# Kernel tuning notes

Measured on AMD Instinct MI355X. Metric: run time of the kernel, lower is better.

The kernel has to match this reference:

```python
import jax, jax.numpy as jnp
import numpy as np
import math

D_MODEL = 512

def setup_inputs() -> dict:
    key = jax.random.key(0)
    k1, k2, k3 = jax.random.split(key, 3)
    X = jax.random.normal(k1, (4, 8192, D_MODEL), dtype=jnp.float32)
    # nn.Linear(d, d, bias=False) weights, applied as x @ W.T
    s = 1.0 / math.sqrt(D_MODEL)
    W_v = jax.random.uniform(k2, (D_MODEL, D_MODEL), dtype=jnp.float32, minval=-s, maxval=s)
    W_theta = jax.random.uniform(k3, (D_MODEL, D_MODEL), dtype=jnp.float32, minval=-s, maxval=s)
    return {"X": X, "W_v": W_v, "W_theta": W_theta}

def reference(X, W_v, W_theta):
    # X: [B, n, d]
    n = X.shape[1]
    d = X.shape[2]
    XW_v = X @ W_v.T            # [B, n, d]
    theta_X = X @ W_theta.T     # [B, n, d]
    # first term: (1/n) * ones(n,n) @ XW_v == column mean broadcast over rows
    first_term = jnp.mean(XW_v, axis=1, keepdims=True)  # [B, 1, d], broadcasts
    # second term: (1/(n*sqrt(d))) * (X @ theta_X^T) @ XW_v
    # associativity-reduced: theta_X^T @ XW_v is [B, d, d]
    kv = jnp.einsum('bnd,bne->bde', theta_X, XW_v)       # [B, d, d]
    second_term = (X @ kv) / (n * math.sqrt(d))          # [B, n, d]
    return first_term + second_term
```

## Files before the change

### kernel.cpp

```cpp
#include <hip/hip_runtime.h>
#include <stdint.h>


typedef __bf16 bf16x8 __attribute__((ext_vector_type(8)));
typedef float f32x4 __attribute__((ext_vector_type(4)));
typedef unsigned short u16x4 __attribute__((ext_vector_type(4)));
typedef unsigned short u16x8 __attribute__((ext_vector_type(8)));

#define BM 128
#define BN 128
#define BK 32

__device__ __forceinline__ unsigned short f2bf(float f) {
  union { float f; unsigned int u; } c; c.f = f;
  unsigned int u = c.u;
  return (unsigned short)((u + 0x7FFFu + ((u >> 16) & 1u)) >> 16);
}
__device__ __forceinline__ float bf2f(unsigned short h) {
  union { unsigned int u; float f; } c; c.u = ((unsigned int)h) << 16;
  return c.f;
}

__device__ __forceinline__ void gld16(const void* g, void* l) {
  using gptr_t = const __attribute__((address_space(1))) void*;
  using lptr_t = __attribute__((address_space(3))) void*;
  __builtin_amdgcn_global_load_lds((gptr_t)(uintptr_t)g,
                                   (lptr_t)(uint32_t)(uintptr_t)l, 16, 0, 0);
}

__device__ __forceinline__ void gemm_tile(const unsigned short* __restrict__ A, int lda,
                                          const unsigned short* __restrict__ B, int ldb,
                                          int K, int m0, int n0, f32x4 (&acc)[4][4]) {
  __shared__ unsigned short sA[BM * BK];
  __shared__ unsigned short sB[BN * BK];
  const int tid = threadIdx.x;
  const int lane = tid & 63;
  const int w = tid >> 6;
  const int wm = w >> 1, wn = w & 1;
  const int quad = lane >> 4, l16 = lane & 15;

#pragma unroll
  for (int mi = 0; mi < 4; mi++)
#pragma unroll
    for (int ni = 0; ni < 4; ni++) acc[mi][ni] = f32x4{0.f, 0.f, 0.f, 0.f};

  for (int kt = 0; kt < K; kt += BK) {
#pragma unroll
    for (int j = 0; j < 2; j++) {
      const int slot = w * 128 + j * 64 + lane;
      const int row = slot >> 2;
      const int col = (slot & 3) * 8;
      gld16(A + (size_t)(m0 + row) * lda + kt + col,
            (char*)sA + (size_t)(w * 128 + j * 64) * 16);
      gld16(B + (size_t)(n0 + row) * ldb + kt + col,
            (char*)sB + (size_t)(w * 128 + j * 64) * 16);
    }
    __syncthreads();

    bf16x8 af[4], bfr[4];
#pragma unroll
    for (int mi = 0; mi < 4; mi++)
      af[mi] = *(const bf16x8*)&sA[(wm * 64 + mi * 16 + l16) * BK + quad * 8];
#pragma unroll
    for (int ni = 0; ni < 4; ni++)
      bfr[ni] = *(const bf16x8*)&sB[(wn * 64 + ni * 16 + l16) * BK + quad * 8];
#pragma unroll
    for (int mi = 0; mi < 4; mi++)
#pragma unroll
      for (int ni = 0; ni < 4; ni++)
        acc[mi][ni] = __builtin_amdgcn_mfma_f32_16x16x32_bf16(af[mi], bfr[ni],
                                                              acc[mi][ni], 0, 0, 0);
    __syncthreads();
  }
}

__global__ __launch_bounds__(256) void prep_kernel(const float* __restrict__ X,
                                                   unsigned short* __restrict__ Xb,
                                                   unsigned short* __restrict__ Xt) {
  __shared__ unsigned short sT[64 * 64];
  const int t = threadIdx.x;
  const int n0 = blockIdx.x * 64, d0 = blockIdx.y * 64;
  const int b = n0 >> 13, nb = n0 & 8191;
  const int r0 = (t >> 4) * 4, c0 = (t & 15) * 4;
  f32x4 v[4];
#pragma unroll
  for (int i = 0; i < 4; i++)
    v[i] = *(const f32x4*)(X + (size_t)(n0 + r0 + i) * 512 + d0 + c0);
#pragma unroll
  for (int i = 0; i < 4; i++) {
    u16x4 o;
#pragma unroll
    for (int j = 0; j < 4; j++) o[j] = f2bf(v[i][j]);
    *(u16x4*)(Xb + (size_t)(n0 + r0 + i) * 512 + d0 + c0) = o;
  }
#pragma unroll
  for (int j = 0; j < 4; j++) {
    u16x4 w;
#pragma unroll
    for (int i = 0; i < 4; i++) w[i] = f2bf(v[i][j]);
    const int c = c0 + j;
    const int rsw = r0 ^ (c & 0x3c);
    *(u16x4*)&sT[c * 64 + rsw] = w;
  }
  __syncthreads();
  const int c = t >> 2, p = t & 3;
  const int sw = c & 0x3c;
  unsigned short* dst = Xt + (size_t)(b * 512 + d0 + c) * 8192 + nb + p * 16;
#pragma unroll
  for (int q = 0; q < 4; q++)
    *(u16x4*)(dst + q * 4) = *(const u16x4*)&sT[c * 64 + ((p * 16 + q * 4) ^ sw)];
}

static __device__ const int TI[10] = {0, 0, 0, 0, 1, 1, 1, 2, 2, 3};
static __device__ const int TJ[10] = {0, 1, 2, 3, 1, 2, 3, 2, 3, 3};

__global__ __launch_bounds__(256) void g_gemm_kernel(const unsigned short* __restrict__ Xt,
                                                     float* __restrict__ G_part) {
  const int t = blockIdx.x;
  const int z = blockIdx.y;
  const int b = z >> 4, s = z & 15;
  const int m0 = TI[t] * 128, n0 = TJ[t] * 128;
  const unsigned short* A = Xt + (size_t)b * 512 * 8192 + (size_t)s * 512;
  f32x4 acc[4][4];
  gemm_tile(A, 8192, A, 8192, 512, m0, n0, acc);
  float* Cp = G_part + ((size_t)z * 10 + t) * 16384;
  const int tid = threadIdx.x, lane = tid & 63, w = tid >> 6;
  const int wm = w >> 1, wn = w & 1, quad = lane >> 4, l16 = lane & 15;
#pragma unroll
  for (int mi = 0; mi < 4; mi++)
#pragma unroll
    for (int ni = 0; ni < 4; ni++) {
      const int ml = wm * 64 + mi * 16 + quad * 4;
      const int nl = wn * 64 + ni * 16 + l16;
      *(f32x4*)(Cp + (size_t)nl * 128 + ml) = acc[mi][ni];
    }
}

__global__ __launch_bounds__(256) void g_fin_kernel(const float* __restrict__ G_part,
                                                    unsigned short* __restrict__ Gb) {
  const int blk = blockIdx.x;
  const int b = blk / 80, rem = blk % 80;
  const int t = rem >> 3, cc = rem & 7;
  const int i = TI[t], j = TJ[t];
  const int m0 = i * 128, n0 = j * 128;
  const int tid = threadIdx.x;
  const int np = cc * 16 + (tid >> 4);
  const int mp = (tid & 15) * 8;
  f32x4 s0 = f32x4{0.f, 0.f, 0.f, 0.f}, s1 = f32x4{0.f, 0.f, 0.f, 0.f};
#pragma unroll
  for (int s = 0; s < 16; s++) {
    const float* p = G_part + (((size_t)(b * 16 + s)) * 10 + t) * 16384 + (size_t)np * 128 + mp;
    s0 += *(const f32x4*)p;
    s1 += *(const f32x4*)(p + 4);
  }
  const float scale = (float)(1.0 / (8192.0 * 22.627416997969522));
  unsigned short h[8];
#pragma unroll
  for (int r = 0; r < 4; r++) { h[r] = f2bf(s0[r] * scale); h[r + 4] = f2bf(s1[r] * scale); }
  unsigned short* Gbb = Gb + (size_t)b * 262144;
#pragma unroll
  for (int r = 0; r < 8; r++)
    Gbb[(size_t)(m0 + mp + r) * 512 + (n0 + np)] = h[r];
  if (i != j) {
    u16x8 o;
#pragma unroll
    for (int r = 0; r < 8; r++) o[r] = h[r];
    *(u16x8*)(Gbb + (size_t)(n0 + np) * 512 + (m0 + mp)) = o;
  }
}

__global__ __launch_bounds__(256) void gemm_rm_kernel(const unsigned short* __restrict__ A,
                                                      const unsigned short* __restrict__ B,
                                                      unsigned short* __restrict__ C,
                                                      size_t Abs, size_t Bbs) {
  const int b = blockIdx.z;
  const int m0 = blockIdx.x * BM, n0 = blockIdx.y * BN;
  f32x4 acc[4][4];
  gemm_tile(A + (size_t)b * Abs, 512, B + (size_t)b * Bbs, 512, 512, m0, n0, acc);
  unsigned short* Cb = C + (size_t)b * 262144;
  const int tid = threadIdx.x, lane = tid & 63, w = tid >> 6;
  const int wm = w >> 1, wn = w & 1, quad = lane >> 4, l16 = lane & 15;
#pragma unroll
  for (int mi = 0; mi < 4; mi++)
#pragma unroll
    for (int ni = 0; ni < 4; ni++) {
      const int m = m0 + wm * 64 + mi * 16 + quad * 4;
      const int n = n0 + wn * 64 + ni * 16 + l16;
#pragma unroll
      for (int r = 0; r < 4; r++)
        Cb[(size_t)(m + r) * 512 + n] = f2bf(acc[mi][ni][r]);
    }
}

__global__ __launch_bounds__(256) void gemm_out_kernel(
    const unsigned short* __restrict__ Xb, const unsigned short* __restrict__ kvt,
    const float* __restrict__ meanV, float* __restrict__ out) {
  const int m0 = blockIdx.x * BM, n0 = blockIdx.y * BN;
  const int b = blockIdx.x >> 6;
  const unsigned short* Bm = kvt + (size_t)b * 262144;
  f32x4 acc[4][4];
  gemm_tile(Xb, 512, Bm, 512, 512, m0, n0, acc);
  const int tid = threadIdx.x, lane = tid & 63, w = tid >> 6;
  const int wm = w >> 1, wn = w & 1, quad = lane >> 4, l16 = lane & 15;
#pragma unroll
  for (int ni = 0; ni < 4; ni++) {
    const int e = n0 + wn * 64 + ni * 16 + l16;
    const float mu = meanV[b * 512 + e];
#pragma unroll
    for (int mi = 0; mi < 4; mi++) {
      const int m = m0 + wm * 64 + mi * 16 + quad * 4;
#pragma unroll
      for (int r = 0; r < 4; r++)
        out[(size_t)(m + r) * 512 + e] = acc[mi][ni][r] + mu;
    }
  }
}

__global__ __launch_bounds__(256) void cast_kernel(const float* __restrict__ in,
                                                   unsigned short* __restrict__ out,
                                                   int n8) {
  const int i = blockIdx.x * 256 + threadIdx.x;
  if (i >= n8) return;
  const f32x4* p = (const f32x4*)(in + (size_t)i * 8);
  f32x4 v0 = p[0], v1 = p[1];
  u16x8 o;
  o[0] = f2bf(v0[0]); o[1] = f2bf(v0[1]); o[2] = f2bf(v0[2]); o[3] = f2bf(v0[3]);
  o[4] = f2bf(v1[0]); o[5] = f2bf(v1[1]); o[6] = f2bf(v1[2]); o[7] = f2bf(v1[3]);
  *(u16x8*)(out + (size_t)i * 8) = o;
}

__global__ __launch_bounds__(256) void meanx_kernel(const unsigned short* __restrict__ Xt,
                                                    float* __restrict__ mean_x) {
  const int be = blockIdx.x;
  const unsigned short* row = Xt + (size_t)be * 8192;
  const int t = threadIdx.x;
  float s = 0.f;
  for (int c = t; c < 1024; c += 256) {
    u16x8 v = *(const u16x8*)(row + c * 8);
#pragma unroll
    for (int j = 0; j < 8; j++) s += bf2f(v[j]);
  }
  __shared__ float red[256];
  red[t] = s;
  __syncthreads();
  for (int st = 128; st > 0; st >>= 1) {
    if (t < st) red[t] += red[t + st];
    __syncthreads();
  }
  if (t == 0) mean_x[be] = red[0] * (1.f / 8192.f);
}

__global__ __launch_bounds__(256) void meanv_kernel(const float* __restrict__ mean_x,
                                                    const float* __restrict__ Wv,
                                                    float* __restrict__ meanV) {
  const int idx = blockIdx.x * 256 + threadIdx.x;
  const int b = idx >> 9, e = idx & 511;
  const float* mx = mean_x + b * 512;
  const float* wr = Wv + (size_t)e * 512;
  float s = 0.f;
  for (int d = 0; d < 512; d += 4) {
    f32x4 a = *(const f32x4*)(mx + d);
    f32x4 w = *(const f32x4*)(wr + d);
    s += a[0] * w[0] + a[1] * w[1] + a[2] * w[2] + a[3] * w[3];
  }
  meanV[idx] = s;
}

extern "C" void kernel_launch(void* const* d_in, const int* in_sizes, int n_in,
                              void* d_out, int out_size, void* d_ws, size_t ws_size,
                              hipStream_t stream) {
  const float* X = (const float*)d_in[0];
  const float* Wv = (const float*)d_in[1];
  const float* Wth = (const float*)d_in[2];
  float* out = (float*)d_out;
  char* ws = (char*)d_ws;

  unsigned short* Xb = (unsigned short*)(ws);
  unsigned short* Xt = (unsigned short*)(ws + 33554432ull);
  float* G_part = (float*)(ws + 67108864ull);
  unsigned short* Gb = (unsigned short*)(ws + 109051904ull);
  unsigned short* Ht = (unsigned short*)(ws + 111149056ull);
  unsigned short* kvt = (unsigned short*)(ws + 113246208ull);
  unsigned short* Wvb = (unsigned short*)(ws + 115343360ull);
  unsigned short* Wtb = (unsigned short*)(ws + 115867648ull);
  float* mean_x = (float*)(ws + 116391936ull);
  float* meanV = (float*)(ws + 116400128ull);

  prep_kernel<<<dim3(512, 8), 256, 0, stream>>>(X, Xb, Xt);
  cast_kernel<<<128, 256, 0, stream>>>(Wv, Wvb, 32768);
  cast_kernel<<<128, 256, 0, stream>>>(Wth, Wtb, 32768);

  g_gemm_kernel<<<dim3(10, 64), 256, 0, stream>>>(Xt, G_part);
  meanx_kernel<<<2048, 256, 0, stream>>>(Xt, mean_x);
  meanv_kernel<<<8, 256, 0, stream>>>(mean_x, Wv, meanV);
  g_fin_kernel<<<320, 256, 0, stream>>>(G_part, Gb);

  gemm_rm_kernel<<<dim3(4, 4, 4), 256, 0, stream>>>(Wvb, Gb, Ht, 0, 262144);
  gemm_rm_kernel<<<dim3(4, 4, 4), 256, 0, stream>>>(Ht, Wtb, kvt, 262144, 0);

  gemm_out_kernel<<<dim3(256, 4), 256, 0, stream>>>(Xb, kvt, meanV, out);
}
```

Before: 261.8 us.

## Fuse column-mean into prep, merge weight casts, double K-step GEMM tile

The column sums of X are now computed inside the prep kernel with wave shuffles and atomics, which removes the separate meanx pass that re-read Xt. The two weight cast kernels are merged into a single launch that also zeroes the mean accumulator. The prep transpose store is widened to 16-byte writes with a different swizzle. The shared GEMM tile now stages two K-chunks per barrier, and diagonal Gram tiles load their operand only once. The costs are extra LDS per block, atomic contention on the mean buffer, and sums taken in fp32 instead of from the bf16 copy.

```diff
diff --git a/kernel.cpp b/kernel.cpp
--- a/kernel.cpp
+++ b/kernel.cpp
@@ -15,10 +15,6 @@
   union { float f; unsigned int u; } c; c.f = f;
   unsigned int u = c.u;
   return (unsigned short)((u + 0x7FFFu + ((u >> 16) & 1u)) >> 16);
-}
-__device__ __forceinline__ float bf2f(unsigned short h) {
-  union { unsigned int u; float f; } c; c.u = ((unsigned int)h) << 16;
-  return c.f;
 }
 
 __device__ __forceinline__ void gld16(const void* g, void* l) {
@@ -30,9 +26,10 @@
 
 __device__ __forceinline__ void gemm_tile(const unsigned short* __restrict__ A, int lda,
                                           const unsigned short* __restrict__ B, int ldb,
-                                          int K, int m0, int n0, f32x4 (&acc)[4][4]) {
-  __shared__ unsigned short sA[BM * BK];
-  __shared__ unsigned short sB[BN * BK];
+                                          int K, int m0, int n0, f32x4 (&acc)[4][4],
+                                          bool sameAB) {
+  __shared__ unsigned short sA[2][BM * BK];
+  __shared__ unsigned short sB[2][BN * BK];
   const int tid = threadIdx.x;
   const int lane = tid & 63;
   const int w = tid >> 6;
@@ -44,39 +41,49 @@
 #pragma unroll
     for (int ni = 0; ni < 4; ni++) acc[mi][ni] = f32x4{0.f, 0.f, 0.f, 0.f};
 
-  for (int kt = 0; kt < K; kt += BK) {
-#pragma unroll
-    for (int j = 0; j < 2; j++) {
-      const int slot = w * 128 + j * 64 + lane;
-      const int row = slot >> 2;
-      const int col = (slot & 3) * 8;
-      gld16(A + (size_t)(m0 + row) * lda + kt + col,
-            (char*)sA + (size_t)(w * 128 + j * 64) * 16);
-      gld16(B + (size_t)(n0 + row) * ldb + kt + col,
-            (char*)sB + (size_t)(w * 128 + j * 64) * 16);
+  for (int kt = 0; kt < K; kt += 2 * BK) {
+#pragma unroll
+    for (int h = 0; h < 2; h++) {
+#pragma unroll
+      for (int j = 0; j < 2; j++) {
+        const int slot = w * 128 + j * 64 + lane;
+        const int row = slot >> 2;
+        const int col = (slot & 3) * 8;
+        const int kc = kt + h * BK + col;
+        gld16(A + (size_t)(m0 + row) * lda + kc,
+              (char*)sA[h] + (size_t)(w * 128 + j * 64) * 16);
+        if (!sameAB)
+          gld16(B + (size_t)(n0 + row) * ldb + kc,
+                (char*)sB[h] + (size_t)(w * 128 + j * 64) * 16);
+      }
     }
     __syncthreads();
 
-    bf16x8 af[4], bfr[4];
-#pragma unroll
-    for (int mi = 0; mi < 4; mi++)
-      af[mi] = *(const bf16x8*)&sA[(wm * 64 + mi * 16 + l16) * BK + quad * 8];
-#pragma unroll
-    for (int ni = 0; ni < 4; ni++)
-      bfr[ni] = *(const bf16x8*)&sB[(wn * 64 + ni * 16 + l16) * BK + quad * 8];
-#pragma unroll
-    for (int mi = 0; mi < 4; mi++)
+#pragma unroll
+    for (int h = 0; h < 2; h++) {
+      const unsigned short* bs = sameAB ? sA[h] : sB[h];
+      bf16x8 af[4], bfr[4];
+#pragma unroll
+      for (int mi = 0; mi < 4; mi++)
+        af[mi] = *(const bf16x8*)&sA[h][(wm * 64 + mi * 16 + l16) * BK + quad * 8];
 #pragma unroll
       for (int ni = 0; ni < 4; ni++)
-        acc[mi][ni] = __builtin_amdgcn_mfma_f32_16x16x32_bf16(af[mi], bfr[ni],
-                                                              acc[mi][ni], 0, 0, 0);
+        bfr[ni] = *(const bf16x8*)&bs[(wn * 64 + ni * 16 + l16) * BK + quad * 8];
+#pragma unroll
+      for (int mi = 0; mi < 4; mi++)
+#pragma unroll
+        for (int ni = 0; ni < 4; ni++)
+          acc[mi][ni] = __builtin_amdgcn_mfma_f32_16x16x32_bf16(af[mi], bfr[ni],
+                                                                acc[mi][ni], 0, 0, 0);
+    }
     __syncthreads();
   }
 }
 
 __global__ __launch_bounds__(256) void prep_kernel(const float* __restrict__ X,
                                                    unsigned short* __restrict__ Xb,
-                                                   unsigned short* __restrict__ Xt) {
+                                                   unsigned short* __restrict__ Xt,
+                                                   float* __restrict__ mean_acc) {
   __shared__ unsigned short sT[64 * 64];
   const int t = threadIdx.x;
   const int n0 = blockIdx.x * 64, d0 = blockIdx.y * 64;
@@ -93,22 +100,61 @@
     for (int j = 0; j < 4; j++) o[j] = f2bf(v[i][j]);
     *(u16x4*)(Xb + (size_t)(n0 + r0 + i) * 512 + d0 + c0) = o;
   }
+  float cs[4];
+#pragma unroll
+  for (int j = 0; j < 4; j++) cs[j] = v[0][j] + v[1][j] + v[2][j] + v[3][j];
 #pragma unroll
   for (int j = 0; j < 4; j++) {
-    u16x4 w;
-#pragma unroll
-    for (int i = 0; i < 4; i++) w[i] = f2bf(v[i][j]);
+    cs[j] += __shfl_xor(cs[j], 16);
+    cs[j] += __shfl_xor(cs[j], 32);
+  }
+  if ((t & 63) < 16) {
+#pragma unroll
+    for (int j = 0; j < 4; j++)
+      atomicAdd(mean_acc + b * 512 + d0 + c0 + j, cs[j]);
+  }
+#pragma unroll
+  for (int j = 0; j < 4; j++) {
+    u16x4 wv;
+#pragma unroll
+    for (int i = 0; i < 4; i++) wv[i] = f2bf(v[i][j]);
     const int c = c0 + j;
-    const int rsw = r0 ^ (c & 0x3c);
-    *(u16x4*)&sT[c * 64 + rsw] = w;
+    const int rsw = r0 ^ (c & 0x38);
+    *(u16x4*)&sT[c * 64 + rsw] = wv;
   }
   __syncthreads();
-  const int c = t >> 2, p = t & 3;
-  const int sw = c & 0x3c;
-  unsigned short* dst = Xt + (size_t)(b * 512 + d0 + c) * 8192 + nb + p * 16;
-#pragma unroll
-  for (int q = 0; q < 4; q++)
-    *(u16x4*)(dst + q * 4) = *(const u16x4*)&sT[c * 64 + ((p * 16 + q * 4) ^ sw)];
+  const int cr = t >> 3, p = t & 7;
+#pragma unroll
+  for (int h = 0; h < 2; h++) {
+    const int c = cr + h * 32;
+    const int phys = (p * 8) ^ (c & 0x38);
+    u16x8 val = *(const u16x8*)&sT[c * 64 + phys];
+    *(u16x8*)(Xt + (size_t)(b * 512 + d0 + c) * 8192 + nb + p * 8) = val;
+  }
+}
+
+__global__ __launch_bounds__(256) void prep_w_kernel(const float* __restrict__ Wv,
+                                                     const float* __restrict__ Wth,
+                                                     unsigned short* __restrict__ Wvb,
+                                                     unsigned short* __restrict__ Wtb,
+                                                     float* __restrict__ mean_acc) {
+  const int blk = blockIdx.x;
+  const int t = threadIdx.x;
+  if (blk == 256) {
+    f32x4 z = f32x4{0.f, 0.f, 0.f, 0.f};
+    *(f32x4*)(mean_acc + t * 8) = z;
+    *(f32x4*)(mean_acc + t * 8 + 4) = z;
+    return;
+  }
+  const float* src = (blk < 128) ? Wv : Wth;
+  unsigned short* dst = (blk < 128) ? Wvb : Wtb;
+  const int i = (blk & 127) * 256 + t;
+  const f32x4* pp = (const f32x4*)(src + (size_t)i * 8);
+  f32x4 v0 = pp[0], v1 = pp[1];
+  u16x8 o;
+  o[0] = f2bf(v0[0]); o[1] = f2bf(v0[1]); o[2] = f2bf(v0[2]); o[3] = f2bf(v0[3]);
+  o[4] = f2bf(v1[0]); o[5] = f2bf(v1[1]); o[6] = f2bf(v1[2]); o[7] = f2bf(v1[3]);
+  *(u16x8*)(dst + (size_t)i * 8) = o;
 }
 
 static __device__ const int TI[10] = {0, 0, 0, 0, 1, 1, 1, 2, 2, 3};
@@ -122,7 +168,7 @@
   const int m0 = TI[t] * 128, n0 = TJ[t] * 128;
   const unsigned short* A = Xt + (size_t)b * 512 * 8192 + (size_t)s * 512;
   f32x4 acc[4][4];
-  gemm_tile(A, 8192, A, 8192, 512, m0, n0, acc);
+  gemm_tile(A, 8192, A, 8192, 512, m0, n0, acc, m0 == n0);
   float* Cp = G_part + ((size_t)z * 10 + t) * 16384;
   const int tid = threadIdx.x, lane = tid & 63, w = tid >> 6;
   const int wm = w >> 1, wn = w & 1, quad = lane >> 4, l16 = lane & 15;
@@ -176,7 +222,7 @@
   const int b = blockIdx.z;
   const int m0 = blockIdx.x * BM, n0 = blockIdx.y * BN;
   f32x4 acc[4][4];
-  gemm_tile(A + (size_t)b * Abs, 512, B + (size_t)b * Bbs, 512, 512, m0, n0, acc);
+  gemm_tile(A + (size_t)b * Abs, 512, B + (size_t)b * Bbs, 512, 512, m0, n0, acc, false);
   unsigned short* Cb = C + (size_t)b * 262144;
   const int tid = threadIdx.x, lane = tid & 63, w = tid >> 6;
   const int wm = w >> 1, wn = w & 1, quad = lane >> 4, l16 = lane & 15;
@@ -199,7 +245,7 @@
   const int b = blockIdx.x >> 6;
   const unsigned short* Bm = kvt + (size_t)b * 262144;
   f32x4 acc[4][4];
-  gemm_tile(Xb, 512, Bm, 512, 512, m0, n0, acc);
+  gemm_tile(Xb, 512, Bm, 512, 512, m0, n0, acc, false);
   const int tid = threadIdx.x, lane = tid & 63, w = tid >> 6;
   const int wm = w >> 1, wn = w & 1, quad = lane >> 4, l16 = lane & 15;
 #pragma unroll
@@ -216,46 +262,12 @@
   }
 }
 
-__global__ __launch_bounds__(256) void cast_kernel(const float* __restrict__ in,
-                                                   unsigned short* __restrict__ out,
-                                                   int n8) {
-  const int i = blockIdx.x * 256 + threadIdx.x;
-  if (i >= n8) return;
-  const f32x4* p = (const f32x4*)(in + (size_t)i * 8);
-  f32x4 v0 = p[0], v1 = p[1];
-  u16x8 o;
-  o[0] = f2bf(v0[0]); o[1] = f2bf(v0[1]); o[2] = f2bf(v0[2]); o[3] = f2bf(v0[3]);
-  o[4] = f2bf(v1[0]); o[5] = f2bf(v1[1]); o[6] = f2bf(v1[2]); o[7] = f2bf(v1[3]);
-  *(u16x8*)(out + (size_t)i * 8) = o;
-}
-
-__global__ __launch_bounds__(256) void meanx_kernel(const unsigned short* __restrict__ Xt,
-                                                    float* __restrict__ mean_x) {
-  const int be = blockIdx.x;
-  const unsigned short* row = Xt + (size_t)be * 8192;
-  const int t = threadIdx.x;
-  float s = 0.f;
-  for (int c = t; c < 1024; c += 256) {
-    u16x8 v = *(const u16x8*)(row + c * 8);
-#pragma unroll
-    for (int j = 0; j < 8; j++) s += bf2f(v[j]);
-  }
-  __shared__ float red[256];
-  red[t] = s;
-  __syncthreads();
-  for (int st = 128; st > 0; st >>= 1) {
-    if (t < st) red[t] += red[t + st];
-    __syncthreads();
-  }
-  if (t == 0) mean_x[be] = red[0] * (1.f / 8192.f);
-}
-
-__global__ __launch_bounds__(256) void meanv_kernel(const float* __restrict__ mean_x,
+__global__ __launch_bounds__(256) void meanv_kernel(const float* __restrict__ mean_acc,
                                                     const float* __restrict__ Wv,
                                                     float* __restrict__ meanV) {
   const int idx = blockIdx.x * 256 + threadIdx.x;
   const int b = idx >> 9, e = idx & 511;
-  const float* mx = mean_x + b * 512;
+  const float* mx = mean_acc + b * 512;
   const float* wr = Wv + (size_t)e * 512;
   float s = 0.f;
   for (int d = 0; d < 512; d += 4) {
@@ -263,7 +275,7 @@
     f32x4 w = *(const f32x4*)(wr + d);
     s += a[0] * w[0] + a[1] * w[1] + a[2] * w[2] + a[3] * w[3];
   }
-  meanV[idx] = s;
+  meanV[idx] = s * (1.f / 8192.f);
 }
 
 extern "C" void kernel_launch(void* const* d_in, const int* in_sizes, int n_in,
@@ -283,16 +295,14 @@
   unsigned short* kvt = (unsigned short*)(ws + 113246208ull);
   unsigned short* Wvb = (unsigned short*)(ws + 115343360ull);
   unsigned short* Wtb = (unsigned short*)(ws + 115867648ull);
-  float* mean_x = (float*)(ws + 116391936ull);
+  float* mean_acc = (float*)(ws + 116391936ull);
   float* meanV = (float*)(ws + 116400128ull);
 
-  prep_kernel<<<dim3(512, 8), 256, 0, stream>>>(X, Xb, Xt);
-  cast_kernel<<<128, 256, 0, stream>>>(Wv, Wvb, 32768);
-  cast_kernel<<<128, 256, 0, stream>>>(Wth, Wtb, 32768);
+  prep_w_kernel<<<257, 256, 0, stream>>>(Wv, Wth, Wvb, Wtb, mean_acc);
+  prep_kernel<<<dim3(512, 8), 256, 0, stream>>>(X, Xb, Xt, mean_acc);
 
   g_gemm_kernel<<<dim3(10, 64), 256, 0, stream>>>(Xt, G_part);
-  meanx_kernel<<<2048, 256, 0, stream>>>(Xt, mean_x);
-  meanv_kernel<<<8, 256, 0, stream>>>(mean_x, Wv, meanV);
+  meanv_kernel<<<8, 256, 0, stream>>>(mean_acc, Wv, meanV);
   g_fin_kernel<<<320, 256, 0, stream>>>(G_part, Gb);
 
   gemm_rm_kernel<<<dim3(4, 4, 4), 256, 0, stream>>>(Wvb, Gb, Ht, 0, 262144);
```

Measured after the change: 351.7 us. 34.3% more time.
